# Kernel optimization log

Measured on AMD Instinct MI355X. Metric: run time of the kernel, lower is better.

The kernel has to match this reference:

```python
import jax, jax.numpy as jnp
import numpy as np

B, N, DIN, DINNER, DOUT, W = 4, 8192, 512, 512, 512, 128


def setup_inputs() -> dict:
    key = jax.random.key(0)
    k1, k2, k3 = jax.random.split(key, 3)
    x = jax.random.normal(k1, (B, N, DIN), jnp.float32)
    # torch Linear weights: (out_features, in_features)
    w_qkv = jax.random.normal(k2, (3 * DINNER, DIN), jnp.float32) * (DIN ** -0.5)
    w_out = jax.random.normal(k3, (DOUT, DINNER), jnp.float32) * (DINNER ** -0.5)
    b_out = jnp.zeros((DOUT,), jnp.float32)
    return {"x": x, "w_qkv": w_qkv, "w_out": w_out, "b_out": b_out}


def reference(x, w_qkv, w_out, b_out):
    b, n, _ = x.shape
    w = W
    scale = DINNER ** -0.5
    pad = (-n) % w  # pad_to_multiple along seq dim (static)
    xp = jnp.pad(x, ((0, 0), (0, pad), (0, 0)))
    qkv = jnp.einsum('bnd,ed->bne', xp, w_qkv)  # to_qkv, no bias
    q, k, v = jnp.split(qkv, 3, axis=-1)
    win = lambda t: t.reshape(b, -1, w, DINNER)  # b (w n) d -> b w n d
    q, k, v = win(q), win(k), win(v)
    # prepend one zero bucket to k, then overlap prev/current windows.
    kp = jnp.pad(k, ((0, 0), (1, 0), (0, 0), (0, 0)))
    k2 = jnp.concatenate((kp[:, :-1], kp[:, 1:]), axis=2)  # (b, nb, 2w, d)
    # NOTE: source bug replicated — v is also built from k, not v.
    v2 = jnp.concatenate((kp[:, :-1], kp[:, 1:]), axis=2)
    sim = jnp.einsum('bwid,bwjd->bwij', q, k2) * scale  # (b, nb, w, 2w)
    i, j = w, 2 * w
    mask = jnp.triu(jnp.ones((i, j), bool), j - i + 1)
    sim = jnp.where(mask, -jnp.finfo(sim.dtype).max, sim)
    attn = jax.nn.softmax(sim, axis=-1)
    out = jnp.einsum('bwij,bwjd->bwid', attn, v2)
    out = out.reshape(b, -1, DINNER)[:, :n]
    return jnp.einsum('bnd,od->bno', out, w_out) + b_out
```

## Files before the change

kernel.cpp:

```cpp
#include <hip/hip_runtime.h>
#include <cstdint>
#include <cstddef>

typedef float f32x4 __attribute__((ext_vector_type(4)));
typedef short s16x8 __attribute__((ext_vector_type(8)));
typedef short s16x4 __attribute__((ext_vector_type(4)));

#define MFMA_BF16(a, b, c) __builtin_amdgcn_mfma_f32_16x16x32_bf16((a), (b), (c), 0, 0, 0)

#define GLD16(g, l)                                                            \
  __builtin_amdgcn_global_load_lds(                                            \
      (const __attribute__((address_space(1))) void*)(g),                      \
      (__attribute__((address_space(3))) void*)(l), 16, 0, 0)

__device__ __forceinline__ unsigned short f2bf(float f) {
  unsigned int u = __float_as_uint(f);
  u += 0x7FFFu + ((u >> 16) & 1u);
  return (unsigned short)(u >> 16);
}

__device__ __forceinline__ s16x8 cvt8(const float* __restrict__ src) {
  const float4 f0 = *(const float4*)src;
  const float4 f1 = *(const float4*)(src + 4);
  s16x8 h;
  h[0] = (short)f2bf(f0.x); h[1] = (short)f2bf(f0.y);
  h[2] = (short)f2bf(f0.z); h[3] = (short)f2bf(f0.w);
  h[4] = (short)f2bf(f1.x); h[5] = (short)f2bf(f1.y);
  h[6] = (short)f2bf(f1.z); h[7] = (short)f2bf(f1.w);
  return h;
}

#define XN 16777216
#define WQN 524288
#define WON 262144
__global__ __launch_bounds__(256)
void cvt_bf16(const float* __restrict__ x, const float* __restrict__ wqkv,
              const float* __restrict__ wout, unsigned short* __restrict__ xb,
              unsigned short* __restrict__ wb, unsigned short* __restrict__ wob) {
  const size_t i = (size_t)(blockIdx.x * 256 + threadIdx.x) * 8;
  const float* src;
  unsigned short* dst;
  if (i < XN) { src = x + i; dst = xb + i; }
  else if (i < XN + WQN) { src = wqkv + (i - XN); dst = wb + (i - XN); }
  else { src = wout + (i - XN - WQN); dst = wob + (i - XN - WQN); }
  *(s16x8*)dst = cvt8(src);
}

__global__ __launch_bounds__(256)
void gemm_qk(const unsigned short* __restrict__ xb, const unsigned short* __restrict__ wb,
             unsigned short* __restrict__ Q, unsigned short* __restrict__ K) {
  __shared__ unsigned short As[128 * 64];
  __shared__ unsigned short Bs[128 * 64];
  const int t = threadIdx.x;
  const int lane = t & 63, wid = t >> 6;
  const int wm = wid >> 1, wn = wid & 1;
  const int nl = lane & 15, quad = lane >> 4;
  const int m0 = blockIdx.y * 128, n0 = blockIdx.x * 128;
  const int sub = lane >> 3;
  const int lblk = (lane & 7) ^ sub;

  const f32x4 zero = {0.f, 0.f, 0.f, 0.f};
  f32x4 acc[4][4];
#pragma unroll
  for (int i = 0; i < 4; ++i)
#pragma unroll
    for (int j = 0; j < 4; ++j) acc[i][j] = zero;

  const unsigned short* gA = xb + (size_t)(m0 + wid * 32 + sub) * 512 + lblk * 8;
  const unsigned short* gB = wb + (size_t)(n0 + wid * 32 + sub) * 512 + lblk * 8;

  for (int kc = 0; kc < 512; kc += 64) {
#pragma unroll
    for (int ii = 0; ii < 4; ++ii) {
      GLD16(gA + kc + (size_t)(ii * 8) * 512, &As[(wid * 32 + ii * 8) * 64]);
      GLD16(gB + kc + (size_t)(ii * 8) * 512, &Bs[(wid * 32 + ii * 8) * 64]);
    }
    __syncthreads();
#pragma unroll
    for (int ks = 0; ks < 2; ++ks) {
      s16x8 af[4], bf[4];
#pragma unroll
      for (int i = 0; i < 4; ++i)
        af[i] = *(const s16x8*)&As[(wm * 64 + i * 16 + nl) * 64 +
                                   (((ks * 4 + quad) ^ (nl & 7)) * 8)];
#pragma unroll
      for (int j = 0; j < 4; ++j)
        bf[j] = *(const s16x8*)&Bs[(wn * 64 + j * 16 + nl) * 64 +
                                   (((ks * 4 + quad) ^ (nl & 7)) * 8)];
#pragma unroll
      for (int i = 0; i < 4; ++i)
#pragma unroll
        for (int j = 0; j < 4; ++j) acc[i][j] = MFMA_BF16(af[i], bf[j], acc[i][j]);
    }
    __syncthreads();
  }
#pragma unroll
  for (int i = 0; i < 4; ++i) {
    const int mrow = m0 + wm * 64 + i * 16 + quad * 4;
#pragma unroll
    for (int j = 0; j < 4; ++j) {
      const int n = n0 + wn * 64 + j * 16 + nl;
      unsigned short* dst = (n < 512 ? Q : K) + (size_t)mrow * 512 + (n & 511);
#pragma unroll
      for (int r = 0; r < 4; ++r) dst[(size_t)r * 512] = f2bf(acc[i][j][r]);
    }
  }
}

__global__ __launch_bounds__(256)
void gemm_kwt(const unsigned short* __restrict__ K, const unsigned short* __restrict__ wob,
              unsigned short* __restrict__ KWT) {
  __shared__ unsigned short As[128 * 64];
  __shared__ unsigned short Bs[128 * 64];
  const int t = threadIdx.x;
  const int lane = t & 63, wid = t >> 6;
  const int wm = wid >> 1, wn = wid & 1;
  const int nl = lane & 15, quad = lane >> 4;
  const int m0 = blockIdx.y * 128, n0 = blockIdx.x * 128;
  const int sub = lane >> 3, lblk = (lane & 7) ^ sub;

  const f32x4 zero = {0.f, 0.f, 0.f, 0.f};
  f32x4 acc[4][4];
#pragma unroll
  for (int i = 0; i < 4; ++i)
#pragma unroll
    for (int j = 0; j < 4; ++j) acc[i][j] = zero;

  const unsigned short* gA = K + (size_t)(m0 + wid * 32 + sub) * 512 + lblk * 8;
  const unsigned short* gB = wob + (size_t)(n0 + wid * 32 + sub) * 512 + lblk * 8;

  for (int kc = 0; kc < 512; kc += 64) {
#pragma unroll
    for (int ii = 0; ii < 4; ++ii) {
      GLD16(gA + kc + (size_t)(ii * 8) * 512, &As[(wid * 32 + ii * 8) * 64]);
      GLD16(gB + kc + (size_t)(ii * 8) * 512, &Bs[(wid * 32 + ii * 8) * 64]);
    }
    __syncthreads();
#pragma unroll
    for (int ks = 0; ks < 2; ++ks) {
      s16x8 af[4], bf[4];
#pragma unroll
      for (int i = 0; i < 4; ++i)
        af[i] = *(const s16x8*)&As[(wm * 64 + i * 16 + nl) * 64 +
                                   (((ks * 4 + quad) ^ (nl & 7)) * 8)];
#pragma unroll
      for (int j = 0; j < 4; ++j)
        bf[j] = *(const s16x8*)&Bs[(wn * 64 + j * 16 + nl) * 64 +
                                   (((ks * 4 + quad) ^ (nl & 7)) * 8)];
#pragma unroll
      for (int i = 0; i < 4; ++i)
#pragma unroll
        for (int j = 0; j < 4; ++j) acc[i][j] = MFMA_BF16(af[i], bf[j], acc[i][j]);
    }
    __syncthreads();
  }
#pragma unroll
  for (int i = 0; i < 4; ++i) {
    const int m = m0 + wm * 64 + i * 16 + quad * 4;
    const int b = m >> 13, ns = m & 8191;
#pragma unroll
    for (int j = 0; j < 4; ++j) {
      const int o = n0 + wn * 64 + j * 16 + nl;
      s16x4 h;
#pragma unroll
      for (int r = 0; r < 4; ++r) h[r] = (short)f2bf(acc[i][j][r]);
      *(s16x4*)&KWT[(size_t)(b * 512 + o) * 8192 + ns] = h;
    }
  }
}

__global__ __launch_bounds__(512)
void attn_p(const unsigned short* __restrict__ Q, const unsigned short* __restrict__ K,
            unsigned short* __restrict__ P) {
  __shared__ unsigned short Qs[128 * 64];
  __shared__ unsigned short Ks[256 * 64];
  __shared__ float redm[128 * 4];
  __shared__ float reds[128 * 4];
  const int t = threadIdx.x;
  const int bx = blockIdx.x, b = bx >> 6, w = bx & 63;
  const int lane = t & 63, wid = t >> 6;
  const int wm = wid >> 2, wn = wid & 3;
  const int nl = lane & 15, quad = lane >> 4;
  const int sub = lane >> 3, lblk = (lane & 7) ^ sub;

  const f32x4 zero = {0.f, 0.f, 0.f, 0.f};
  f32x4 acc[4][4];
#pragma unroll
  for (int i = 0; i < 4; ++i)
#pragma unroll
    for (int j = 0; j < 4; ++j) acc[i][j] = zero;

  const unsigned short* Qb = Q + (size_t)(b * 8192 + w * 128) * 512;
  const unsigned short* Kb = K + (size_t)(b * 8192) * 512;

  for (int kc = 0; kc < 512; kc += 64) {
#pragma unroll
    for (int ii = 0; ii < 2; ++ii)
      GLD16(Qb + (size_t)(wid * 16 + ii * 8 + sub) * 512 + kc + lblk * 8,
            &Qs[(wid * 16 + ii * 8) * 64]);
#pragma unroll
    for (int ii = 0; ii < 4; ++ii) {
      int sq = w * 128 - 128 + wid * 32 + ii * 8 + sub;
      if (sq < 0) sq = 0;
      GLD16(Kb + (size_t)sq * 512 + kc + lblk * 8, &Ks[(wid * 32 + ii * 8) * 64]);
    }
    __syncthreads();
#pragma unroll
    for (int ks = 0; ks < 2; ++ks) {
      s16x8 af[4], bf[4];
#pragma unroll
      for (int i = 0; i < 4; ++i)
        af[i] = *(const s16x8*)&Qs[(wm * 64 + i * 16 + nl) * 64 +
                                   (((ks * 4 + quad) ^ (nl & 7)) * 8)];
#pragma unroll
      for (int j = 0; j < 4; ++j)
        bf[j] = *(const s16x8*)&Ks[(wn * 64 + j * 16 + nl) * 64 +
                                   (((ks * 4 + quad) ^ (nl & 7)) * 8)];
#pragma unroll
      for (int i = 0; i < 4; ++i)
#pragma unroll
        for (int j = 0; j < 4; ++j) acc[i][j] = MFMA_BF16(af[i], bf[j], acc[i][j]);
    }
    __syncthreads();
  }

  const float scale = 0.04419417382415922f;
  float rmax[4][4];
#pragma unroll
  for (int i = 0; i < 4; ++i) {
#pragma unroll
    for (int r = 0; r < 4; ++r) {
      const int row = wm * 64 + i * 16 + quad * 4 + r;
      float mx = -3.4e38f;
#pragma unroll
      for (int j = 0; j < 4; ++j) {
        const int col = wn * 64 + j * 16 + nl;
        float v = acc[i][j][r] * scale;
        if (col >= 128 && col - 128 > row) v = -3.0e38f;
        if (w == 0 && col < 128) v = 0.0f;
        acc[i][j][r] = v;
        mx = fmaxf(mx, v);
      }
      rmax[i][r] = mx;
    }
  }
#pragma unroll
  for (int off = 1; off < 16; off <<= 1)
#pragma unroll
    for (int i = 0; i < 4; ++i)
#pragma unroll
      for (int r = 0; r < 4; ++r)
        rmax[i][r] = fmaxf(rmax[i][r], __shfl_xor(rmax[i][r], off, 64));
  if (nl == 0) {
#pragma unroll
    for (int i = 0; i < 4; ++i)
#pragma unroll
      for (int r = 0; r < 4; ++r)
        redm[(wm * 64 + i * 16 + quad * 4 + r) * 4 + wn] = rmax[i][r];
  }
  __syncthreads();
  float rsum[4][4];
#pragma unroll
  for (int i = 0; i < 4; ++i) {
#pragma unroll
    for (int r = 0; r < 4; ++r) {
      const f32x4 mv = *(const f32x4*)&redm[(wm * 64 + i * 16 + quad * 4 + r) * 4];
      const float m = fmaxf(fmaxf(mv[0], mv[1]), fmaxf(mv[2], mv[3]));
      float s = 0.f;
#pragma unroll
      for (int j = 0; j < 4; ++j) {
        const float p = __expf(acc[i][j][r] - m);
        acc[i][j][r] = p;
        s += p;
      }
      rsum[i][r] = s;
    }
  }
#pragma unroll
  for (int off = 1; off < 16; off <<= 1)
#pragma unroll
    for (int i = 0; i < 4; ++i)
#pragma unroll
      for (int r = 0; r < 4; ++r) rsum[i][r] += __shfl_xor(rsum[i][r], off, 64);
  if (nl == 0) {
#pragma unroll
    for (int i = 0; i < 4; ++i)
#pragma unroll
      for (int r = 0; r < 4; ++r)
        reds[(wm * 64 + i * 16 + quad * 4 + r) * 4 + wn] = rsum[i][r];
  }
  __syncthreads();
#pragma unroll
  for (int i = 0; i < 4; ++i) {
#pragma unroll
    for (int r = 0; r < 4; ++r) {
      const int row = wm * 64 + i * 16 + quad * 4 + r;
      const f32x4 sv = *(const f32x4*)&reds[row * 4];
      const float inv = 1.0f / (sv[0] + sv[1] + sv[2] + sv[3]);
#pragma unroll
      for (int j = 0; j < 4; ++j) {
        const int col = wn * 64 + j * 16 + nl;
        float pv = acc[i][j][r] * inv;
        if (w == 0 && col < 128) pv = 0.0f;
        P[(size_t)bx * 32768 + (size_t)row * 256 + col] = f2bf(pv);
      }
    }
  }
}

__global__ __launch_bounds__(512)
void gemm_out(const unsigned short* __restrict__ P, const unsigned short* __restrict__ KWT,
              const float* __restrict__ bias, float* __restrict__ out) {
  __shared__ unsigned short As[128 * 64];
  __shared__ unsigned short Bs[256 * 64];
  const int t = threadIdx.x;
  const int wbx = blockIdx.y, b = wbx >> 6, w = wbx & 63;
  const int o0 = blockIdx.x * 256;
  const int lane = t & 63, wid = t >> 6;
  const int wm = wid >> 2, wn = wid & 3;
  const int nl = lane & 15, quad = lane >> 4;
  const int sub = lane >> 3, lblk = (lane & 7) ^ sub;

  const f32x4 zero = {0.f, 0.f, 0.f, 0.f};
  f32x4 acc[4][4];
#pragma unroll
  for (int i = 0; i < 4; ++i)
#pragma unroll
    for (int j = 0; j < 4; ++j) acc[i][j] = zero;

  const unsigned short* Pw = P + (size_t)wbx * 32768;
  const int seqbase = w * 128 - 128;

  for (int kc = 0; kc < 256; kc += 64) {
#pragma unroll
    for (int ii = 0; ii < 2; ++ii)
      GLD16(Pw + (size_t)(wid * 16 + ii * 8 + sub) * 256 + kc + lblk * 8,
            &As[(wid * 16 + ii * 8) * 64]);
    int sq = seqbase + kc + lblk * 8;
    if (sq < 0) sq = 0;
#pragma unroll
    for (int ii = 0; ii < 4; ++ii)
      GLD16(KWT + (size_t)(b * 512 + o0 + wid * 32 + ii * 8 + sub) * 8192 + sq,
            &Bs[(wid * 32 + ii * 8) * 64]);
    __syncthreads();
#pragma unroll
    for (int ks = 0; ks < 2; ++ks) {
      s16x8 af[4], bf[4];
#pragma unroll
      for (int i = 0; i < 4; ++i)
        af[i] = *(const s16x8*)&As[(wm * 64 + i * 16 + nl) * 64 +
                                   (((ks * 4 + quad) ^ (nl & 7)) * 8)];
#pragma unroll
      for (int j = 0; j < 4; ++j)
        bf[j] = *(const s16x8*)&Bs[(wn * 64 + j * 16 + nl) * 64 +
                                   (((ks * 4 + quad) ^ (nl & 7)) * 8)];
#pragma unroll
      for (int i = 0; i < 4; ++i)
#pragma unroll
        for (int j = 0; j < 4; ++j) acc[i][j] = MFMA_BF16(af[i], bf[j], acc[i][j]);
    }
    __syncthreads();
  }
#pragma unroll
  for (int i = 0; i < 4; ++i) {
    const int row = wm * 64 + i * 16 + quad * 4;
#pragma unroll
    for (int j = 0; j < 4; ++j) {
      const int o = o0 + wn * 64 + j * 16 + nl;
      const float bo = bias[o];
      float* dst = out + (size_t)(b * 8192 + w * 128 + row) * 512 + o;
#pragma unroll
      for (int r = 0; r < 4; ++r) dst[(size_t)r * 512] = acc[i][j][r] + bo;
    }
  }
}

extern "C" void kernel_launch(void* const* d_in, const int* in_sizes, int n_in,
                              void* d_out, int out_size, void* d_ws, size_t ws_size,
                              hipStream_t stream) {
  const float* x = (const float*)d_in[0];
  const float* w_qkv = (const float*)d_in[1];
  const float* w_out = (const float*)d_in[2];
  const float* b_out = (const float*)d_in[3];
  float* out = (float*)d_out;

  char* ws = (char*)d_ws;
  unsigned short* Q = (unsigned short*)ws;
  unsigned short* K = (unsigned short*)(ws + (size_t)33554432);
  unsigned short* xb = (unsigned short*)(ws + (size_t)67108864);
  unsigned short* KWT = (unsigned short*)(ws + (size_t)67108864);
  unsigned short* P = (unsigned short*)(ws + (size_t)100663296);
  unsigned short* wb = (unsigned short*)(ws + (size_t)100663296);
  unsigned short* wob = (unsigned short*)(ws + (size_t)100663296 + 1048576);

  cvt_bf16<<<dim3(8576), dim3(256), 0, stream>>>(x, w_qkv, w_out, xb, wb, wob);
  gemm_qk<<<dim3(8, 256), dim3(256), 0, stream>>>(xb, wb, Q, K);
  gemm_kwt<<<dim3(4, 256), dim3(256), 0, stream>>>(K, wob, KWT);
  attn_p<<<dim3(256), dim3(512), 0, stream>>>(Q, K, P);
  gemm_out<<<dim3(2, 256), dim3(512), 0, stream>>>(P, KWT, b_out, out);
}
```

Baseline: 262.4 us.

## Fold Wout into K weights, fuse x conversion into GEMM, fuse attention with output projection

Precomputes Wout·Wk as extra weight rows, so K·Wout^T comes straight from x in the same GEMM that produces Q and K. The fp32 x is now converted to bf16 inside the GEMM tile load instead of in a separate pass. The attention probabilities stay in LDS and are multiplied directly by KWT tiles, which removes the P round-trip through global memory and one launch. It also adds XCD-aware block mapping and a transposed MFMA operand order for vectorised Q/K stores. In exchange it reassociates the bf16 rounding of the weight product and adds branchy code paths.

```diff
diff --git a/kernel.cpp b/kernel.cpp
--- a/kernel.cpp
+++ b/kernel.cpp
@@ -30,34 +30,22 @@
   return h;
 }
 
-#define XN 16777216
-#define WQN 524288
-#define WON 262144
 __global__ __launch_bounds__(256)
-void cvt_bf16(const float* __restrict__ x, const float* __restrict__ wqkv,
-              const float* __restrict__ wout, unsigned short* __restrict__ xb,
-              unsigned short* __restrict__ wb, unsigned short* __restrict__ wob) {
+void wcvt(const float* __restrict__ wqkv, unsigned short* __restrict__ Wcat) {
   const size_t i = (size_t)(blockIdx.x * 256 + threadIdx.x) * 8;
-  const float* src;
-  unsigned short* dst;
-  if (i < XN) { src = x + i; dst = xb + i; }
-  else if (i < XN + WQN) { src = wqkv + (i - XN); dst = wb + (i - XN); }
-  else { src = wout + (i - XN - WQN); dst = wob + (i - XN - WQN); }
-  *(s16x8*)dst = cvt8(src);
+  *(s16x8*)(Wcat + i) = cvt8(wqkv + i);
 }
 
 __global__ __launch_bounds__(256)
-void gemm_qk(const unsigned short* __restrict__ xb, const unsigned short* __restrict__ wb,
-             unsigned short* __restrict__ Q, unsigned short* __restrict__ K) {
-  __shared__ unsigned short As[128 * 64];
-  __shared__ unsigned short Bs[128 * 64];
-  const int t = threadIdx.x;
-  const int lane = t & 63, wid = t >> 6;
+void wprod(const float* __restrict__ wqkv, const float* __restrict__ wout,
+           unsigned short* __restrict__ Wcat) {
+  __shared__ unsigned short As[128 * 72];
+  __shared__ unsigned short Bs[128 * 72];
+  const int t = threadIdx.x, lane = t & 63, wid = t >> 6;
   const int wm = wid >> 1, wn = wid & 1;
   const int nl = lane & 15, quad = lane >> 4;
-  const int m0 = blockIdx.y * 128, n0 = blockIdx.x * 128;
-  const int sub = lane >> 3;
-  const int lblk = (lane & 7) ^ sub;
+  const int o0 = blockIdx.x * 128, c0 = blockIdx.y * 128;
+  const int srow = t >> 3, scol = (t & 7) * 8;
 
   const f32x4 zero = {0.f, 0.f, 0.f, 0.f};
   f32x4 acc[4][4];
@@ -66,14 +54,26 @@
 #pragma unroll
     for (int j = 0; j < 4; ++j) acc[i][j] = zero;
 
-  const unsigned short* gA = xb + (size_t)(m0 + wid * 32 + sub) * 512 + lblk * 8;
-  const unsigned short* gB = wb + (size_t)(n0 + wid * 32 + sub) * 512 + lblk * 8;
-
   for (int kc = 0; kc < 512; kc += 64) {
 #pragma unroll
-    for (int ii = 0; ii < 4; ++ii) {
-      GLD16(gA + kc + (size_t)(ii * 8) * 512, &As[(wid * 32 + ii * 8) * 64]);
-      GLD16(gB + kc + (size_t)(ii * 8) * 512, &Bs[(wid * 32 + ii * 8) * 64]);
+    for (int p = 0; p < 4; ++p) {
+      const int r = srow + p * 32;
+      *(s16x8*)&As[r * 72 + scol] = cvt8(wout + (size_t)(o0 + r) * 512 + kc + scol);
+    }
+#pragma unroll
+    for (int p = 0; p < 4; ++p) {
+      const int dloc = p * 16 + (t >> 4);
+      const int cbase = (t & 15) * 8;
+      const float4 f0 = *(const float4*)(wqkv + (size_t)(512 + kc + dloc) * 512 + c0 + cbase);
+      const float4 f1 = *(const float4*)(wqkv + (size_t)(512 + kc + dloc) * 512 + c0 + cbase + 4);
+      Bs[(cbase + 0) * 72 + dloc] = f2bf(f0.x);
+      Bs[(cbase + 1) * 72 + dloc] = f2bf(f0.y);
+      Bs[(cbase + 2) * 72 + dloc] = f2bf(f0.z);
+      Bs[(cbase + 3) * 72 + dloc] = f2bf(f0.w);
+      Bs[(cbase + 4) * 72 + dloc] = f2bf(f1.x);
+      Bs[(cbase + 5) * 72 + dloc] = f2bf(f1.y);
+      Bs[(cbase + 6) * 72 + dloc] = f2bf(f1.z);
+      Bs[(cbase + 7) * 72 + dloc] = f2bf(f1.w);
     }
     __syncthreads();
 #pragma unroll
@@ -81,12 +81,10 @@
       s16x8 af[4], bf[4];
 #pragma unroll
       for (int i = 0; i < 4; ++i)
-        af[i] = *(const s16x8*)&As[(wm * 64 + i * 16 + nl) * 64 +
-                                   (((ks * 4 + quad) ^ (nl & 7)) * 8)];
+        af[i] = *(const s16x8*)&As[(wm * 64 + i * 16 + nl) * 72 + ks * 32 + quad * 8];
 #pragma unroll
       for (int j = 0; j < 4; ++j)
-        bf[j] = *(const s16x8*)&Bs[(wn * 64 + j * 16 + nl) * 64 +
-                                   (((ks * 4 + quad) ^ (nl & 7)) * 8)];
+        bf[j] = *(const s16x8*)&Bs[(wn * 64 + j * 16 + nl) * 72 + ks * 32 + quad * 8];
 #pragma unroll
       for (int i = 0; i < 4; ++i)
 #pragma unroll
@@ -96,28 +94,33 @@
   }
 #pragma unroll
   for (int i = 0; i < 4; ++i) {
-    const int mrow = m0 + wm * 64 + i * 16 + quad * 4;
+    const int o = o0 + wm * 64 + i * 16 + quad * 4;
 #pragma unroll
     for (int j = 0; j < 4; ++j) {
-      const int n = n0 + wn * 64 + j * 16 + nl;
-      unsigned short* dst = (n < 512 ? Q : K) + (size_t)mrow * 512 + (n & 511);
-#pragma unroll
-      for (int r = 0; r < 4; ++r) dst[(size_t)r * 512] = f2bf(acc[i][j][r]);
+      const int c = c0 + wn * 64 + j * 16 + nl;
+#pragma unroll
+      for (int r = 0; r < 4; ++r)
+        Wcat[(size_t)(1024 + o + r) * 512 + c] = f2bf(acc[i][j][r]);
     }
   }
 }
 
 __global__ __launch_bounds__(256)
-void gemm_kwt(const unsigned short* __restrict__ K, const unsigned short* __restrict__ wob,
+void gemm_qkw(const float* __restrict__ x, const unsigned short* __restrict__ Wcat,
+              unsigned short* __restrict__ Q, unsigned short* __restrict__ K,
               unsigned short* __restrict__ KWT) {
   __shared__ unsigned short As[128 * 64];
   __shared__ unsigned short Bs[128 * 64];
-  const int t = threadIdx.x;
-  const int lane = t & 63, wid = t >> 6;
+  const int t = threadIdx.x, lane = t & 63, wid = t >> 6;
   const int wm = wid >> 1, wn = wid & 1;
   const int nl = lane & 15, quad = lane >> 4;
-  const int m0 = blockIdx.y * 128, n0 = blockIdx.x * 128;
   const int sub = lane >> 3, lblk = (lane & 7) ^ sub;
+  const int l = blockIdx.x;
+  const int xcd = l & 7, g = l >> 3;
+  const int mt = (g / 12) * 8 + xcd, nt = g - (g / 12) * 12;
+  const int m0 = mt * 128, n0 = nt * 128;
+  const bool qk = nt < 8;
+  const int srow = t >> 3, scol8 = t & 7;
 
   const f32x4 zero = {0.f, 0.f, 0.f, 0.f};
   f32x4 acc[4][4];
@@ -126,56 +129,98 @@
 #pragma unroll
     for (int j = 0; j < 4; ++j) acc[i][j] = zero;
 
-  const unsigned short* gA = K + (size_t)(m0 + wid * 32 + sub) * 512 + lblk * 8;
-  const unsigned short* gB = wob + (size_t)(n0 + wid * 32 + sub) * 512 + lblk * 8;
+  const unsigned short* gB = Wcat + (size_t)(n0 + wid * 32 + sub) * 512 + lblk * 8;
 
   for (int kc = 0; kc < 512; kc += 64) {
 #pragma unroll
-    for (int ii = 0; ii < 4; ++ii) {
-      GLD16(gA + kc + (size_t)(ii * 8) * 512, &As[(wid * 32 + ii * 8) * 64]);
+    for (int ii = 0; ii < 4; ++ii)
       GLD16(gB + kc + (size_t)(ii * 8) * 512, &Bs[(wid * 32 + ii * 8) * 64]);
-    }
-    __syncthreads();
-#pragma unroll
-    for (int ks = 0; ks < 2; ++ks) {
-      s16x8 af[4], bf[4];
-#pragma unroll
-      for (int i = 0; i < 4; ++i)
-        af[i] = *(const s16x8*)&As[(wm * 64 + i * 16 + nl) * 64 +
-                                   (((ks * 4 + quad) ^ (nl & 7)) * 8)];
-#pragma unroll
-      for (int j = 0; j < 4; ++j)
-        bf[j] = *(const s16x8*)&Bs[(wn * 64 + j * 16 + nl) * 64 +
-                                   (((ks * 4 + quad) ^ (nl & 7)) * 8)];
-#pragma unroll
-      for (int i = 0; i < 4; ++i)
-#pragma unroll
-        for (int j = 0; j < 4; ++j) acc[i][j] = MFMA_BF16(af[i], bf[j], acc[i][j]);
-    }
-    __syncthreads();
-  }
-#pragma unroll
-  for (int i = 0; i < 4; ++i) {
-    const int m = m0 + wm * 64 + i * 16 + quad * 4;
-    const int b = m >> 13, ns = m & 8191;
-#pragma unroll
-    for (int j = 0; j < 4; ++j) {
-      const int o = n0 + wn * 64 + j * 16 + nl;
-      s16x4 h;
-#pragma unroll
-      for (int r = 0; r < 4; ++r) h[r] = (short)f2bf(acc[i][j][r]);
-      *(s16x4*)&KWT[(size_t)(b * 512 + o) * 8192 + ns] = h;
+#pragma unroll
+    for (int p = 0; p < 4; ++p) {
+      const int r = srow + p * 32;
+      const s16x8 h = cvt8(x + (size_t)(m0 + r) * 512 + kc + scol8 * 8);
+      *(s16x8*)&As[r * 64 + ((scol8 ^ (r & 7)) << 3)] = h;
+    }
+    __syncthreads();
+    if (qk) {
+#pragma unroll
+      for (int ks = 0; ks < 2; ++ks) {
+        s16x8 af[4], bf[4];
+#pragma unroll
+        for (int i = 0; i < 4; ++i)
+          af[i] = *(const s16x8*)&As[(wm * 64 + i * 16 + nl) * 64 +
+                                     (((ks * 4 + quad) ^ (nl & 7)) * 8)];
+#pragma unroll
+        for (int j = 0; j < 4; ++j)
+          bf[j] = *(const s16x8*)&Bs[(wn * 64 + j * 16 + nl) * 64 +
+                                     (((ks * 4 + quad) ^ (nl & 7)) * 8)];
+#pragma unroll
+        for (int i = 0; i < 4; ++i)
+#pragma unroll
+          for (int j = 0; j < 4; ++j) acc[i][j] = MFMA_BF16(bf[j], af[i], acc[i][j]);
+      }
+    } else {
+#pragma unroll
+      for (int ks = 0; ks < 2; ++ks) {
+        s16x8 af[4], bf[4];
+#pragma unroll
+        for (int i = 0; i < 4; ++i)
+          af[i] = *(const s16x8*)&As[(wm * 64 + i * 16 + nl) * 64 +
+                                     (((ks * 4 + quad) ^ (nl & 7)) * 8)];
+#pragma unroll
+        for (int j = 0; j < 4; ++j)
+          bf[j] = *(const s16x8*)&Bs[(wn * 64 + j * 16 + nl) * 64 +
+                                     (((ks * 4 + quad) ^ (nl & 7)) * 8)];
+#pragma unroll
+        for (int i = 0; i < 4; ++i)
+#pragma unroll
+          for (int j = 0; j < 4; ++j) acc[i][j] = MFMA_BF16(af[i], bf[j], acc[i][j]);
+      }
+    }
+    __syncthreads();
+  }
+  if (qk) {
+#pragma unroll
+    for (int i = 0; i < 4; ++i) {
+      const int m = m0 + wm * 64 + i * 16 + nl;
+#pragma unroll
+      for (int j = 0; j < 4; ++j) {
+        const int n = n0 + wn * 64 + j * 16 + quad * 4;
+        unsigned short* dst = (n < 512 ? Q : K) + (size_t)m * 512 + (n & 511);
+        s16x4 h;
+#pragma unroll
+        for (int r = 0; r < 4; ++r) h[r] = (short)f2bf(acc[i][j][r]);
+        *(s16x4*)dst = h;
+      }
+    }
+  } else {
+#pragma unroll
+    for (int i = 0; i < 4; ++i) {
+      const int ms = m0 + wm * 64 + i * 16 + quad * 4;
+      const int b = ms >> 13, ns = ms & 8191;
+#pragma unroll
+      for (int j = 0; j < 4; ++j) {
+        const int o = n0 - 1024 + wn * 64 + j * 16 + nl;
+        s16x4 h;
+#pragma unroll
+        for (int r = 0; r < 4; ++r) h[r] = (short)f2bf(acc[i][j][r]);
+        *(s16x4*)&KWT[(size_t)(b * 512 + o) * 8192 + ns] = h;
+      }
     }
   }
 }
 
 __global__ __launch_bounds__(512)
-void attn_p(const unsigned short* __restrict__ Q, const unsigned short* __restrict__ K,
-            unsigned short* __restrict__ P) {
-  __shared__ unsigned short Qs[128 * 64];
-  __shared__ unsigned short Ks[256 * 64];
-  __shared__ float redm[128 * 4];
-  __shared__ float reds[128 * 4];
+void attn_out(const unsigned short* __restrict__ Q, const unsigned short* __restrict__ K,
+              const unsigned short* __restrict__ KWT, const float* __restrict__ bias,
+              float* __restrict__ out) {
+  __shared__ char smem[81920];
+  unsigned short* Qs = (unsigned short*)smem;
+  unsigned short* Ks = (unsigned short*)(smem + 16384);
+  unsigned short* Ps = (unsigned short*)smem;
+  unsigned short* Bs2 = (unsigned short*)(smem + 65536);
+  __shared__ float redm[512];
+  __shared__ float reds[512];
   const int t = threadIdx.x;
   const int bx = blockIdx.x, b = bx >> 6, w = bx & 63;
   const int lane = t & 63, wid = t >> 6;
@@ -302,75 +347,61 @@
         const int col = wn * 64 + j * 16 + nl;
         float pv = acc[i][j][r] * inv;
         if (w == 0 && col < 128) pv = 0.0f;
-        P[(size_t)bx * 32768 + (size_t)row * 256 + col] = f2bf(pv);
-      }
-    }
-  }
-}
-
-__global__ __launch_bounds__(512)
-void gemm_out(const unsigned short* __restrict__ P, const unsigned short* __restrict__ KWT,
-              const float* __restrict__ bias, float* __restrict__ out) {
-  __shared__ unsigned short As[128 * 64];
-  __shared__ unsigned short Bs[256 * 64];
-  const int t = threadIdx.x;
-  const int wbx = blockIdx.y, b = wbx >> 6, w = wbx & 63;
-  const int o0 = blockIdx.x * 256;
-  const int lane = t & 63, wid = t >> 6;
-  const int wm = wid >> 2, wn = wid & 3;
-  const int nl = lane & 15, quad = lane >> 4;
-  const int sub = lane >> 3, lblk = (lane & 7) ^ sub;
-
-  const f32x4 zero = {0.f, 0.f, 0.f, 0.f};
-  f32x4 acc[4][4];
-#pragma unroll
-  for (int i = 0; i < 4; ++i)
-#pragma unroll
-    for (int j = 0; j < 4; ++j) acc[i][j] = zero;
-
-  const unsigned short* Pw = P + (size_t)wbx * 32768;
+        const int cb = col >> 3;
+        Ps[row * 256 + (((cb ^ (row & 7)) << 3) | (col & 7))] = f2bf(pv);
+      }
+    }
+  }
+  __syncthreads();
+
   const int seqbase = w * 128 - 128;
-
-  for (int kc = 0; kc < 256; kc += 64) {
-#pragma unroll
-    for (int ii = 0; ii < 2; ++ii)
-      GLD16(Pw + (size_t)(wid * 16 + ii * 8 + sub) * 256 + kc + lblk * 8,
-            &As[(wid * 16 + ii * 8) * 64]);
-    int sq = seqbase + kc + lblk * 8;
-    if (sq < 0) sq = 0;
-#pragma unroll
-    for (int ii = 0; ii < 4; ++ii)
-      GLD16(KWT + (size_t)(b * 512 + o0 + wid * 32 + ii * 8 + sub) * 8192 + sq,
-            &Bs[(wid * 32 + ii * 8) * 64]);
-    __syncthreads();
-#pragma unroll
-    for (int ks = 0; ks < 2; ++ks) {
-      s16x8 af[4], bf[4];
-#pragma unroll
-      for (int i = 0; i < 4; ++i)
-        af[i] = *(const s16x8*)&As[(wm * 64 + i * 16 + nl) * 64 +
-                                   (((ks * 4 + quad) ^ (nl & 7)) * 8)];
-#pragma unroll
-      for (int j = 0; j < 4; ++j)
-        bf[j] = *(const s16x8*)&Bs[(wn * 64 + j * 16 + nl) * 64 +
-                                   (((ks * 4 + quad) ^ (nl & 7)) * 8)];
-#pragma unroll
-      for (int i = 0; i < 4; ++i)
-#pragma unroll
-        for (int j = 0; j < 4; ++j) acc[i][j] = MFMA_BF16(af[i], bf[j], acc[i][j]);
-    }
-    __syncthreads();
-  }
-#pragma unroll
-  for (int i = 0; i < 4; ++i) {
-    const int row = wm * 64 + i * 16 + quad * 4;
-#pragma unroll
-    for (int j = 0; j < 4; ++j) {
-      const int o = o0 + wn * 64 + j * 16 + nl;
-      const float bo = bias[o];
-      float* dst = out + (size_t)(b * 8192 + w * 128 + row) * 512 + o;
-#pragma unroll
-      for (int r = 0; r < 4; ++r) dst[(size_t)r * 512] = acc[i][j][r] + bo;
+#pragma unroll 1
+  for (int och = 0; och < 4; ++och) {
+    f32x4 acc2[4][2];
+#pragma unroll
+    for (int i = 0; i < 4; ++i)
+#pragma unroll
+      for (int j = 0; j < 2; ++j) acc2[i][j] = zero;
+#pragma unroll 1
+    for (int kch = 0; kch < 4; ++kch) {
+#pragma unroll
+      for (int ii = 0; ii < 2; ++ii) {
+        const int orow = och * 128 + wid * 16 + ii * 8 + sub;
+        int sq = seqbase + kch * 64 + lblk * 8;
+        if (sq < 0) sq = 0;
+        GLD16(KWT + (size_t)(b * 512 + orow) * 8192 + sq, &Bs2[(wid * 16 + ii * 8) * 64]);
+      }
+      __syncthreads();
+#pragma unroll
+      for (int ks = 0; ks < 2; ++ks) {
+        const int kb = kch * 8 + ks * 4 + quad;
+        s16x8 af[4], bf[2];
+#pragma unroll
+        for (int i = 0; i < 4; ++i)
+          af[i] = *(const s16x8*)&Ps[(wm * 64 + i * 16 + nl) * 256 +
+                                     (((kb ^ (nl & 7)) << 3))];
+#pragma unroll
+        for (int j = 0; j < 2; ++j)
+          bf[j] = *(const s16x8*)&Bs2[(wn * 32 + j * 16 + nl) * 64 +
+                                      (((ks * 4 + quad) ^ (nl & 7)) * 8)];
+#pragma unroll
+        for (int i = 0; i < 4; ++i)
+#pragma unroll
+          for (int j = 0; j < 2; ++j) acc2[i][j] = MFMA_BF16(af[i], bf[j], acc2[i][j]);
+      }
+      __syncthreads();
+    }
+#pragma unroll
+    for (int i = 0; i < 4; ++i) {
+      const int mrow = wm * 64 + i * 16 + quad * 4;
+      float* dst = out + (size_t)(b * 8192 + w * 128 + mrow) * 512;
+#pragma unroll
+      for (int j = 0; j < 2; ++j) {
+        const int o = och * 128 + wn * 32 + j * 16 + nl;
+        const float bo = bias[o];
+#pragma unroll
+        for (int r = 0; r < 4; ++r) dst[(size_t)r * 512 + o] = acc2[i][j][r] + bo;
+      }
     }
   }
 }
@@ -387,15 +418,11 @@
   char* ws = (char*)d_ws;
   unsigned short* Q = (unsigned short*)ws;
   unsigned short* K = (unsigned short*)(ws + (size_t)33554432);
-  unsigned short* xb = (unsigned short*)(ws + (size_t)67108864);
   unsigned short* KWT = (unsigned short*)(ws + (size_t)67108864);
-  unsigned short* P = (unsigned short*)(ws + (size_t)100663296);
-  unsigned short* wb = (unsigned short*)(ws + (size_t)100663296);
-  unsigned short* wob = (unsigned short*)(ws + (size_t)100663296 + 1048576);
-
-  cvt_bf16<<<dim3(8576), dim3(256), 0, stream>>>(x, w_qkv, w_out, xb, wb, wob);
-  gemm_qk<<<dim3(8, 256), dim3(256), 0, stream>>>(xb, wb, Q, K);
-  gemm_kwt<<<dim3(4, 256), dim3(256), 0, stream>>>(K, wob, KWT);
-  attn_p<<<dim3(256), dim3(512), 0, stream>>>(Q, K, P);
-  gemm_out<<<dim3(2, 256), dim3(512), 0, stream>>>(P, KWT, b_out, out);
-}
+  unsigned short* Wcat = (unsigned short*)(ws + (size_t)100663296);
+
+  wcvt<<<dim3(256), dim3(256), 0, stream>>>(w_qkv, Wcat);
+  wprod<<<dim3(4, 4), dim3(256), 0, stream>>>(w_qkv, w_out, Wcat);
+  gemm_qkw<<<dim3(3072), dim3(256), 0, stream>>>(x, Wcat, Q, K, KWT);
+  attn_out<<<dim3(256), dim3(512), 0, stream>>>(Q, K, KWT, b_out, out);
+}
```

New measurement: 372.3 us. 41.9% more time.
